# Optimization experiments

Hardware: AMD Instinct MI355X
Metric: run time of the kernel (lower is better)

Reference implementation:

```python
import jax, jax.numpy as jnp
import numpy as np

KERNEL_MUL = 2.0
KERNEL_NUM = 5


def setup_inputs() -> dict:
    key = jax.random.key(0)
    k1, k2 = jax.random.split(key)
    source = jax.random.normal(k1, (4096, 256), dtype=jnp.float32)
    target = jax.random.normal(k2, (4096, 256), dtype=jnp.float32)
    return {"source": source, "target": target}


def _mmd(source, target):
    b = source.shape[0]
    total = jnp.concatenate([source, target], axis=0)  # [N, D], N = 2b
    n = total.shape[0]
    sq = jnp.sum(total * total, axis=-1)               # [N]
    gram = total @ total.T                             # [N, N]
    L2 = sq[:, None] + sq[None, :] - 2.0 * gram        # [N, N]
    # Data-dependent bandwidth (original uses .data -> no grad through it)
    bandwidth = jax.lax.stop_gradient(jnp.sum(L2) / (n * n - n))
    # Multi-bandwidth RBF kernel, averaged over KERNEL_NUM geometric sigmas.
    kernels = jnp.zeros_like(L2)
    for i in range(KERNEL_NUM):
        sigma = bandwidth * (KERNEL_MUL ** i)
        kernels = kernels + jnp.exp(-L2 / sigma)
    kernels = kernels / KERNEL_NUM
    XX = kernels[:b, :b]
    YY = kernels[b:, b:]
    XY = kernels[:b, b:]
    YX = kernels[b:, :b]
    return jnp.mean(XX + YY - XY - YX)


def reference(source, target):
    return _mmd(source, target)
```

## Files before the change

kernel.cpp:

```cpp
#include <hip/hip_runtime.h>
#include <hip/hip_bf16.h>

#define N_TOTAL 8192
#define B_HALF  4096
#define D       256
#define BM      128
#define NTILES  (N_TOTAL / BM)
#define NBLK    (NTILES * (NTILES + 1) / 2)
#define PREP_BLOCKS (N_TOTAL / 32)

typedef __bf16 bf16x8v __attribute__((ext_vector_type(8)));
typedef float  f32x4v  __attribute__((ext_vector_type(4)));

__device__ __forceinline__ unsigned short f2bf(float x) {
    unsigned int u = __float_as_uint(x);
    return (unsigned short)((u + 0x7FFFu + ((u >> 16) & 1u)) >> 16);
}
__device__ __forceinline__ float bf2f(unsigned short b) {
    return __uint_as_float(((unsigned int)b) << 16);
}

__global__ void prep_kernel(const float* __restrict__ src,
                            const float* __restrict__ tgt,
                            unsigned short* __restrict__ tb2,
                            float* __restrict__ sq,
                            float* __restrict__ colsum_part,
                            double* __restrict__ sumsq_part)
{
    __shared__ float colpart[4][256];
    __shared__ double wsum[4];
    int tid = threadIdx.x;
    int wv = tid >> 6, ln = tid & 63;
    int row0 = blockIdx.x * 32 + wv * 8;

    float cp0 = 0.f, cp1 = 0.f, cp2 = 0.f, cp3 = 0.f;
    double dsum = 0.0;

    for (int t = 0; t < 8; ++t) {
        int row = row0 + t;
        const float* p = (row < B_HALF) ? (src + (size_t)row * D)
                                        : (tgt + (size_t)(row - B_HALF) * D);
        float4 v = *(const float4*)(p + ln * 4);
        unsigned short b0 = f2bf(v.x), b1 = f2bf(v.y), b2 = f2bf(v.z), b3 = f2bf(v.w);
        float x0 = bf2f(b0), x1 = bf2f(b1), x2 = bf2f(b2), x3 = bf2f(b3);
        ushort4 u; u.x = b0; u.y = b1; u.z = b2; u.w = b3;
        *(ushort4*)(tb2 + ((size_t)(ln >> 1) * N_TOTAL + row) * 8 + (ln & 1) * 4) = u;

        cp0 += x0; cp1 += x1; cp2 += x2; cp3 += x3;

        float sqp = x0 * x0 + x1 * x1 + x2 * x2 + x3 * x3;
        #pragma unroll
        for (int off = 32; off; off >>= 1) sqp += __shfl_down(sqp, off, 64);
        if (ln == 0) { sq[row] = sqp; dsum += (double)sqp; }
    }
    colpart[wv][ln * 4 + 0] = cp0;
    colpart[wv][ln * 4 + 1] = cp1;
    colpart[wv][ln * 4 + 2] = cp2;
    colpart[wv][ln * 4 + 3] = cp3;
    if (ln == 0) wsum[wv] = dsum;
    __syncthreads();
    colsum_part[blockIdx.x * 256 + tid] =
        colpart[0][tid] + colpart[1][tid] + colpart[2][tid] + colpart[3][tid];
    if (tid == 0)
        sumsq_part[blockIdx.x] = wsum[0] + wsum[1] + wsum[2] + wsum[3];
}

__global__ void bw_kernel(const float* __restrict__ colsum_part,
                          const double* __restrict__ sumsq_part,
                          float* __restrict__ cexp) {
    __shared__ double red1[256], red2[256];
    int tid = threadIdx.x;
    float cs = 0.f;
    #pragma unroll 8
    for (int b = 0; b < PREP_BLOCKS; ++b)
        cs += colsum_part[b * 256 + tid];
    red1[tid] = sumsq_part[tid];
    red2[tid] = (double)cs * (double)cs;
    __syncthreads();
    for (int off = 128; off; off >>= 1) {
        if (tid < off) { red1[tid] += red1[tid + off]; red2[tid] += red2[tid + off]; }
        __syncthreads();
    }
    if (tid == 0) {
        double sl2 = 2.0 * (double)N_TOTAL * red1[0] - 2.0 * red2[0];
        double bw = sl2 / ((double)N_TOTAL * N_TOTAL - (double)N_TOTAL);
        cexp[0] = (float)(1.4426950408889634 / (16.0 * bw));
    }
}

__global__ __launch_bounds__(256)
void mmd_kernel(const unsigned short* __restrict__ tb2,
                const float* __restrict__ sq,
                const float* __restrict__ cexp_p,
                double* __restrict__ partials) {
    __shared__ float sqi[BM], sqj[BM];
    __shared__ float redbuf[4];

    int t = blockIdx.x;
    int r = (int)((sqrtf(8.0f * (float)t + 1.0f) - 1.0f) * 0.5f);
    while ((r + 1) * (r + 2) / 2 <= t) ++r;
    while (r * (r + 1) / 2 > t) --r;
    int c = t - r * (r + 1) / 2;
    int rowBase = r * BM, colBase = c * BM;

    int tid = threadIdx.x;
    int wv = tid >> 6, ln = tid & 63;
    int wr = wv >> 1, wc = wv & 1;
    int lo = ln & 15, hi = ln >> 4;

    if (tid < BM) sqi[tid] = sq[rowBase + tid];
    else          sqj[tid - BM] = sq[colBase + (tid - BM)];
    float cexp = cexp_p[0];
    __syncthreads();

    const char* pa = (const char*)tb2 +
        ((size_t)hi * N_TOTAL + rowBase + wr * 64 + lo) * 16;
    const char* pb = (const char*)tb2 +
        ((size_t)hi * N_TOTAL + colBase + wc * 64 + lo) * 16;
    const size_t KKSTRIDE = (size_t)4 * N_TOTAL * 16;

    f32x4v acc[4][4] = {};
    bf16x8v a[2][4], b[2][4];

    #pragma unroll
    for (int mi = 0; mi < 4; ++mi) a[0][mi] = *(const bf16x8v*)(pa + mi * 256);
    #pragma unroll
    for (int ni = 0; ni < 4; ++ni) b[0][ni] = *(const bf16x8v*)(pb + ni * 256);

    #pragma unroll
    for (int kk = 0; kk < 8; ++kk) {
        const int cur = kk & 1, nxt = cur ^ 1;
        if (kk < 7) {
            const char* qa = pa + (size_t)(kk + 1) * KKSTRIDE;
            const char* qb = pb + (size_t)(kk + 1) * KKSTRIDE;
            #pragma unroll
            for (int mi = 0; mi < 4; ++mi)
                a[nxt][mi] = *(const bf16x8v*)(qa + mi * 256);
            #pragma unroll
            for (int ni = 0; ni < 4; ++ni)
                b[nxt][ni] = *(const bf16x8v*)(qb + ni * 256);
        }
        #pragma unroll
        for (int mi = 0; mi < 4; ++mi)
            #pragma unroll
            for (int ni = 0; ni < 4; ++ni)
                acc[mi][ni] = __builtin_amdgcn_mfma_f32_16x16x32_bf16(
                    a[cur][mi], b[cur][ni], acc[mi][ni], 0, 0, 0);
    }

    float tacc = 0.f;
    #pragma unroll
    for (int mi = 0; mi < 4; ++mi) {
        float si4[4];
        #pragma unroll
        for (int rg = 0; rg < 4; ++rg)
            si4[rg] = sqi[wr * 64 + mi * 16 + hi * 4 + rg];
        #pragma unroll
        for (int ni = 0; ni < 4; ++ni) {
            float sj = sqj[wc * 64 + ni * 16 + lo];
            #pragma unroll
            for (int rg = 0; rg < 4; ++rg) {
                float arg = (2.0f * acc[mi][ni][rg] - (si4[rg] + sj)) * cexp;
                float e0 = __builtin_amdgcn_exp2f(arg);
                float e2 = e0 * e0, e4 = e2 * e2, e8 = e4 * e4, e16 = e8 * e8;
                tacc += (e0 + e2) + ((e4 + e8) + e16);
            }
        }
    }
    float w = ((r < NTILES / 2) == (c < NTILES / 2)) ? 1.f : -1.f;
    if (r != c) w *= 2.f;
    tacc *= w;

    #pragma unroll
    for (int off = 32; off; off >>= 1) tacc += __shfl_down(tacc, off, 64);
    if (ln == 0) redbuf[wv] = tacc;
    __syncthreads();
    if (tid == 0)
        partials[blockIdx.x] =
            (double)(redbuf[0] + redbuf[1] + redbuf[2] + redbuf[3]);
}

__global__ void final_kernel(const double* __restrict__ partials,
                             float* __restrict__ out) {
    __shared__ double dred[256];
    int tid = threadIdx.x;
    double d = 0.0;
    for (int i = tid; i < NBLK; i += 256) d += partials[i];
    dred[tid] = d;
    __syncthreads();
    for (int off = 128; off; off >>= 1) {
        if (tid < off) dred[tid] += dred[tid + off];
        __syncthreads();
    }
    if (tid == 0)
        out[0] = (float)(dred[0] / (5.0 * (double)B_HALF * (double)B_HALF));
}

extern "C" void kernel_launch(void* const* d_in, const int* in_sizes, int n_in,
                              void* d_out, int out_size, void* d_ws, size_t ws_size,
                              hipStream_t stream) {
    const float* src = (const float*)d_in[0];
    const float* tgt = (const float*)d_in[1];
    float* out = (float*)d_out;
    char* ws = (char*)d_ws;

    float*  cexp     = (float*)(ws + 16);
    double* ssqpart  = (double*)(ws + 2048);
    float*  sq       = (float*)(ws + 4096);
    double* partials = (double*)(ws + 36864);
    float*  cspart   = (float*)(ws + 131072);
    unsigned short* tb2 = (unsigned short*)(ws + 1048576);

    prep_kernel<<<PREP_BLOCKS, 256, 0, stream>>>(src, tgt, tb2, sq, cspart,
                                                 ssqpart);
    bw_kernel<<<1, 256, 0, stream>>>(cspart, ssqpart, cexp);
    mmd_kernel<<<NBLK, 256, 0, stream>>>(tb2, sq, cexp, partials);
    final_kernel<<<1, 256, 0, stream>>>(partials, out);
}
```

Before: 59.85 us.

## Fuse bandwidth reduction into prep, remap tile order, pack epilogue math

```diff
diff --git a/kernel.cpp b/kernel.cpp
--- a/kernel.cpp
+++ b/kernel.cpp
@@ -11,6 +11,7 @@
 
 typedef __bf16 bf16x8v __attribute__((ext_vector_type(8)));
 typedef float  f32x4v  __attribute__((ext_vector_type(4)));
+typedef float  f32x2v  __attribute__((ext_vector_type(2)));
 
 __device__ __forceinline__ unsigned short f2bf(float x) {
     unsigned int u = __float_as_uint(x);
@@ -25,10 +26,13 @@
                             unsigned short* __restrict__ tb2,
                             float* __restrict__ sq,
                             float* __restrict__ colsum_part,
-                            double* __restrict__ sumsq_part)
-{
+                            double* __restrict__ sumsq_part,
+                            unsigned int* __restrict__ counter,
+                            float* __restrict__ cexp) {
     __shared__ float colpart[4][256];
     __shared__ double wsum[4];
+    __shared__ double red1[256], red2[256];
+    __shared__ int lastFlag;
     int tid = threadIdx.x;
     int wv = tid >> 6, ln = tid & 63;
     int row0 = blockIdx.x * 32 + wv * 8;
@@ -61,42 +65,44 @@
     __syncthreads();
     colsum_part[blockIdx.x * 256 + tid] =
         colpart[0][tid] + colpart[1][tid] + colpart[2][tid] + colpart[3][tid];
-    if (tid == 0)
+    if (tid == 0) {
         sumsq_part[blockIdx.x] = wsum[0] + wsum[1] + wsum[2] + wsum[3];
-}
-
-__global__ void bw_kernel(const float* __restrict__ colsum_part,
-                          const double* __restrict__ sumsq_part,
-                          float* __restrict__ cexp) {
-    __shared__ double red1[256], red2[256];
-    int tid = threadIdx.x;
-    float cs = 0.f;
-    #pragma unroll 8
-    for (int b = 0; b < PREP_BLOCKS; ++b)
-        cs += colsum_part[b * 256 + tid];
-    red1[tid] = sumsq_part[tid];
-    red2[tid] = (double)cs * (double)cs;
-    __syncthreads();
-    for (int off = 128; off; off >>= 1) {
-        if (tid < off) { red1[tid] += red1[tid + off]; red2[tid] += red2[tid + off]; }
+        __threadfence();
+        unsigned int old = atomicAdd(counter, 1u);
+        lastFlag = ((old & (PREP_BLOCKS - 1)) == PREP_BLOCKS - 1);
+    }
+    __syncthreads();
+    if (lastFlag) {
+        __threadfence();
+        float cs = 0.f;
+        #pragma unroll 8
+        for (int b = 0; b < PREP_BLOCKS; ++b)
+            cs += colsum_part[b * 256 + tid];
+        red1[tid] = sumsq_part[tid];
+        red2[tid] = (double)cs * (double)cs;
         __syncthreads();
-    }
-    if (tid == 0) {
-        double sl2 = 2.0 * (double)N_TOTAL * red1[0] - 2.0 * red2[0];
-        double bw = sl2 / ((double)N_TOTAL * N_TOTAL - (double)N_TOTAL);
-        cexp[0] = (float)(1.4426950408889634 / (16.0 * bw));
-    }
-}
-
-__global__ __launch_bounds__(256)
+        for (int off = 128; off; off >>= 1) {
+            if (tid < off) { red1[tid] += red1[tid + off]; red2[tid] += red2[tid + off]; }
+            __syncthreads();
+        }
+        if (tid == 0) {
+            double sl2 = 2.0 * (double)N_TOTAL * red1[0] - 2.0 * red2[0];
+            double bw = sl2 / ((double)N_TOTAL * N_TOTAL - (double)N_TOTAL);
+            cexp[0] = (float)(1.4426950408889634 / (16.0 * bw));
+        }
+    }
+}
+
+__global__ __launch_bounds__(256, 3)
 void mmd_kernel(const unsigned short* __restrict__ tb2,
                 const float* __restrict__ sq,
                 const float* __restrict__ cexp_p,
                 double* __restrict__ partials) {
-    __shared__ float sqi[BM], sqj[BM];
+    __shared__ float nsqi[BM], nsqj[BM];
     __shared__ float redbuf[4];
 
-    int t = blockIdx.x;
+    int bid = blockIdx.x;
+    int t = (bid & 7) * (NBLK / 8) + (bid >> 3);
     int r = (int)((sqrtf(8.0f * (float)t + 1.0f) - 1.0f) * 0.5f);
     while ((r + 1) * (r + 2) / 2 <= t) ++r;
     while (r * (r + 1) / 2 > t) --r;
@@ -108,9 +114,9 @@
     int wr = wv >> 1, wc = wv & 1;
     int lo = ln & 15, hi = ln >> 4;
 
-    if (tid < BM) sqi[tid] = sq[rowBase + tid];
-    else          sqj[tid - BM] = sq[colBase + (tid - BM)];
     float cexp = cexp_p[0];
+    if (tid < BM) nsqi[tid] = -sq[rowBase + tid] * cexp;
+    else          nsqj[tid - BM] = -sq[colBase + (tid - BM)] * cexp;
     __syncthreads();
 
     const char* pa = (const char*)tb2 +
@@ -140,33 +146,45 @@
             for (int ni = 0; ni < 4; ++ni)
                 b[nxt][ni] = *(const bf16x8v*)(qb + ni * 256);
         }
+        __builtin_amdgcn_s_setprio(1);
         #pragma unroll
         for (int mi = 0; mi < 4; ++mi)
             #pragma unroll
             for (int ni = 0; ni < 4; ++ni)
                 acc[mi][ni] = __builtin_amdgcn_mfma_f32_16x16x32_bf16(
                     a[cur][mi], b[cur][ni], acc[mi][ni], 0, 0, 0);
-    }
-
-    float tacc = 0.f;
+        __builtin_amdgcn_s_setprio(0);
+    }
+
+    float c2 = 2.0f * cexp;
+    f32x2v c2v = {c2, c2};
+    f32x2v t0 = {0.f, 0.f}, t1 = {0.f, 0.f};
     #pragma unroll
     for (int mi = 0; mi < 4; ++mi) {
-        float si4[4];
-        #pragma unroll
-        for (int rg = 0; rg < 4; ++rg)
-            si4[rg] = sqi[wr * 64 + mi * 16 + hi * 4 + rg];
+        int rb = wr * 64 + mi * 16 + hi * 4;
+        f32x2v siA = {nsqi[rb + 0], nsqi[rb + 1]};
+        f32x2v siB = {nsqi[rb + 2], nsqi[rb + 3]};
         #pragma unroll
         for (int ni = 0; ni < 4; ++ni) {
-            float sj = sqj[wc * 64 + ni * 16 + lo];
-            #pragma unroll
-            for (int rg = 0; rg < 4; ++rg) {
-                float arg = (2.0f * acc[mi][ni][rg] - (si4[rg] + sj)) * cexp;
-                float e0 = __builtin_amdgcn_exp2f(arg);
-                float e2 = e0 * e0, e4 = e2 * e2, e8 = e4 * e4, e16 = e8 * e8;
-                tacc += (e0 + e2) + ((e4 + e8) + e16);
-            }
-        }
-    }
+            float nsj = nsqj[wc * 64 + ni * 16 + lo];
+            f32x2v njv = {nsj, nsj};
+            f32x2v sA = siA + njv, sB = siB + njv;
+            f32x2v gA = {acc[mi][ni][0], acc[mi][ni][1]};
+            f32x2v gB = {acc[mi][ni][2], acc[mi][ni][3]};
+            f32x2v aA = gA * c2v + sA;
+            f32x2v aB = gB * c2v + sB;
+            f32x2v eA, eB;
+            eA[0] = __builtin_amdgcn_exp2f(aA[0]);
+            eA[1] = __builtin_amdgcn_exp2f(aA[1]);
+            eB[0] = __builtin_amdgcn_exp2f(aB[0]);
+            eB[1] = __builtin_amdgcn_exp2f(aB[1]);
+            f32x2v e2A = eA * eA, e4A = e2A * e2A, e8A = e4A * e4A, e16A = e8A * e8A;
+            f32x2v e2B = eB * eB, e4B = e2B * e2B, e8B = e4B * e4B, e16B = e8B * e8B;
+            t0 += (eA + e2A) + ((e4A + e8A) + e16A);
+            t1 += (eB + e2B) + ((e4B + e8B) + e16B);
+        }
+    }
+    float tacc = (t0[0] + t0[1]) + (t1[0] + t1[1]);
     float w = ((r < NTILES / 2) == (c < NTILES / 2)) ? 1.f : -1.f;
     if (r != c) w *= 2.f;
     tacc *= w;
@@ -176,7 +194,7 @@
     if (ln == 0) redbuf[wv] = tacc;
     __syncthreads();
     if (tid == 0)
-        partials[blockIdx.x] =
+        partials[bid] =
             (double)(redbuf[0] + redbuf[1] + redbuf[2] + redbuf[3]);
 }
 
@@ -204,6 +222,7 @@
     float* out = (float*)d_out;
     char* ws = (char*)d_ws;
 
+    unsigned int* counter = (unsigned int*)(ws + 0);
     float*  cexp     = (float*)(ws + 16);
     double* ssqpart  = (double*)(ws + 2048);
     float*  sq       = (float*)(ws + 4096);
@@ -212,8 +231,7 @@
     unsigned short* tb2 = (unsigned short*)(ws + 1048576);
 
     prep_kernel<<<PREP_BLOCKS, 256, 0, stream>>>(src, tgt, tb2, sq, cspart,
-                                                 ssqpart);
-    bw_kernel<<<1, 256, 0, stream>>>(cspart, ssqpart, cexp);
+                                                 ssqpart, counter, cexp);
     mmd_kernel<<<NBLK, 256, 0, stream>>>(tb2, sq, cexp, partials);
     final_kernel<<<1, 256, 0, stream>>>(partials, out);
 }
```

Measured after the change: 59.68 us. Within noise of the previous version (-0.3%).
